# Kernel optimization log

Measured on AMD Instinct MI355X. Metric: run time of the kernel, lower is better.

Reference implementation:

```python
import jax, jax.numpy as jnp
import numpy as np

B, S, HID, H, D = 4, 1024, 2048, 16, 128
ROT = D // 2  # GLM 2D rotary: rotary dim is half the head dim (64)


def _rope_tables(seq_len, dim, base=10000.0):
    # dim = ROT; inv_freq over dim//2 frequencies, emb = cat(freqs, freqs)
    inv_freq = 1.0 / (base ** (jnp.arange(0, dim, 2, dtype=jnp.float32) / dim))
    t = jnp.arange(seq_len, dtype=jnp.float32)
    freqs = jnp.einsum('s,f->sf', t, inv_freq)          # [S, dim//2]
    emb = jnp.concatenate([freqs, freqs], axis=-1)       # [S, dim]
    return jnp.cos(emb), jnp.sin(emb)


def _rotate_half(x):
    x1, x2 = jnp.split(x, 2, axis=-1)
    return jnp.concatenate([-x2, x1], axis=-1)


def _apply_rope(x, cos, sin, pos_id):
    # x: [B,H,S,ROT]; pos_id: [B,S]; tables: [S,ROT]
    c = cos[pos_id][:, None, :, :]  # [B,1,S,ROT]
    s = sin[pos_id][:, None, :, :]
    return x * c + _rotate_half(x) * s


def setup_inputs() -> dict:
    key = jax.random.key(0)
    ks = jax.random.split(key, 12)
    w = 0.02
    inp = {
        'query': jax.random.normal(ks[0], (B, S, HID), jnp.float32),
        'key': jax.random.normal(ks[1], (B, S, HID), jnp.float32),
        'value': jax.random.normal(ks[2], (B, S, HID), jnp.float32),
        'mask': jnp.zeros((B, 1, S, S), jnp.float32),
        'position_bias': jax.random.normal(ks[3], (1, H, S, S), jnp.float32) * 0.1,
        'prev_attn': jax.random.normal(ks[4], (B, H, S, S), jnp.float32) * 0.1,
        'position_ids': jax.random.randint(ks[5], (B, 2, S), 0, S, jnp.int32),
        'Wq': jax.random.normal(ks[6], (HID, HID), jnp.float32) * w,
        'bq': jnp.zeros((HID,), jnp.float32),
        'Wk': jax.random.normal(ks[7], (HID, HID), jnp.float32) * w,
        'bk': jnp.zeros((HID,), jnp.float32),
        'Wv': jax.random.normal(ks[8], (HID, HID), jnp.float32) * w,
        'bv': jnp.zeros((HID,), jnp.float32),
        'Wo': jax.random.normal(ks[9], (HID, HID), jnp.float32) * w,
        'bo': jnp.zeros((HID,), jnp.float32),
    }
    return inp


def reference(query, key, value, mask, position_bias, prev_attn,
              Wq, bq, Wk, bk, Wv, bv, Wo, bo, position_ids):
    # QKV projections -> [B,H,S,D]
    def proj(x, W, b):
        return (x @ W.T + b).reshape(B, S, H, D).transpose(0, 2, 1, 3)
    q = proj(query, Wq, bq)
    k = proj(key, Wk, bk)
    v = proj(value, Wv, bv)

    # GLM 2D rotary: split head dim in halves, rope each with its own ids
    q1, q2 = jnp.split(q, 2, axis=-1)
    k1, k2 = jnp.split(k, 2, axis=-1)
    cos, sin = _rope_tables(S, ROT)
    pid = position_ids[:, 0, :]        # [B,S]
    bid = position_ids[:, 1, :]        # [B,S]
    q1 = _apply_rope(q1, cos, sin, pid)
    k1 = _apply_rope(k1, cos, sin, pid)
    q2 = _apply_rope(q2, cos, sin, bid)
    k2 = _apply_rope(k2, cos, sin, bid)
    q = jnp.concatenate([q1, q2], axis=-1)
    k = jnp.concatenate([k1, k2], axis=-1)

    scores = jnp.einsum('bhsd,bhtd->bhst', q, k)
    scores = scores + position_bias
    scores = scores / jnp.sqrt(jnp.float32(D))
    scores = scores + mask
    scores = scores + prev_attn          # residual attention accumulation
    prev_attn_out = scores
    probs = jax.nn.softmax(scores, axis=-1)
    ctx = jnp.einsum('bhst,bhtd->bhsd', probs, v)
    ctx = ctx.transpose(0, 2, 1, 3).reshape(B, S, HID)
    out = ctx @ Wo.T + bo
    return out, prev_attn_out
```

## Files before the change

kernel.cpp:

```cpp
#include <hip/hip_runtime.h>


#define B_  4
#define S_  1024
#define HID_ 2048
#define H_  16
#define D_  128
#define RSQRT_D 0.08838834764831845f

typedef _Float16 f16x8 __attribute__((ext_vector_type(8)));
typedef _Float16 f16x4 __attribute__((ext_vector_type(4)));
typedef float f32x4 __attribute__((ext_vector_type(4)));
typedef unsigned int u32x2 __attribute__((ext_vector_type(2)));
typedef unsigned int u32x4 __attribute__((ext_vector_type(4)));

#define MFMA16(a, b, c) __builtin_amdgcn_mfma_f32_16x16x32_f16(a, b, c, 0, 0, 0)

__device__ __forceinline__ void gll16(const void* g, void* l) {
  __builtin_amdgcn_global_load_lds(
      (const __attribute__((address_space(1))) void*)g,
      (__attribute__((address_space(3))) void*)l, 16, 0, 0);
}

__global__ __launch_bounds__(256) void cvt_all_kernel(
    const float* __restrict__ w0, const float* __restrict__ w1,
    const float* __restrict__ w2, const float* __restrict__ w3,
    const float* __restrict__ x0, const float* __restrict__ x1,
    const float* __restrict__ x2,
    _Float16* __restrict__ dw0, _Float16* __restrict__ dw1,
    _Float16* __restrict__ dw2, _Float16* __restrict__ dw3,
    _Float16* __restrict__ dx0, _Float16* __restrict__ dx1,
    _Float16* __restrict__ dx2,
    float* __restrict__ tcos, float* __restrict__ tsin) {
  if (blockIdx.x >= 20480) {
    const int i = (blockIdx.x - 20480) * 256 + threadIdx.x;
    const int pos = i >> 5, j = i & 31;
    const float inv = expf(-(float)j * (9.210340371976184f / 32.0f));
    const float ang = (float)pos * inv;
    tcos[i] = cosf(ang);
    tsin[i] = sinf(ang);
    return;
  }
  const int i = blockIdx.x * blockDim.x + threadIdx.x;
  const float* src;
  _Float16* dst;
  int off;
  if (i < 2097152) {
    const int seg = i >> 19;
    off = i & 524287;
    src = (seg == 0) ? w0 : (seg == 1) ? w1 : (seg == 2) ? w2 : w3;
    dst = (seg == 0) ? dw0 : (seg == 1) ? dw1 : (seg == 2) ? dw2 : dw3;
  } else {
    const int j = i - 2097152;
    const int seg = j >> 20;
    off = j & 1048575;
    src = (seg == 0) ? x0 : (seg == 1) ? x1 : x2;
    dst = (seg == 0) ? dx0 : (seg == 1) ? dx1 : dx2;
  }
  const f32x4* in4 = (const f32x4*)src;
  f32x4 a = in4[(size_t)off * 2], b = in4[(size_t)off * 2 + 1];
  f16x8 v;
  v[0] = (_Float16)a[0]; v[1] = (_Float16)a[1]; v[2] = (_Float16)a[2]; v[3] = (_Float16)a[3];
  v[4] = (_Float16)b[0]; v[5] = (_Float16)b[1]; v[6] = (_Float16)b[2]; v[7] = (_Float16)b[3];
  *(f16x8*)(dst + (size_t)off * 8) = v;
}

__global__ __launch_bounds__(256) void proj_qkv_kernel(
    const _Float16* __restrict__ Xq, const _Float16* __restrict__ Xk,
    const _Float16* __restrict__ Xv,
    const _Float16* __restrict__ Wq, const _Float16* __restrict__ Wk,
    const _Float16* __restrict__ Wv,
    const float* __restrict__ bq, const float* __restrict__ bk,
    const float* __restrict__ bv,
    _Float16* __restrict__ oq, _Float16* __restrict__ ok,
    _Float16* __restrict__ ovt,
    const int* __restrict__ pids, const float* __restrict__ tcos,
    const float* __restrict__ tsin) {
  constexpr int N = HID_, K = HID_;
  constexpr int BK = 64;
  __shared__ _Float16 As[128 * BK];
  __shared__ _Float16 Bs[128 * BK];

  const int tid = threadIdx.x;
  const int gbid = (blockIdx.x & 7) * 192 + (blockIdx.x >> 3);
  const int seg = gbid >> 9;
  const int bid = gbid & 511;
  const _Float16* A  = (seg == 0) ? Xq : (seg == 1) ? Xk : Xv;
  const _Float16* Bw = (seg == 0) ? Wq : (seg == 1) ? Wk : Wv;
  const float*  bias = (seg == 0) ? bq : (seg == 1) ? bk : bv;

  const int tm = bid >> 4, tn = bid & 15;
  const int m0 = tm * 128, n0 = tn * 128;
  const int w = tid >> 6, l = tid & 63;
  const int mw = (w >> 1) * 64, nw = (w & 1) * 64;
  const int lr = l & 15, lh = l >> 4;

  f32x4 acc[4][4] = {};

  for (int kt = 0; kt < K / BK; ++kt) {
    const int k0 = kt * BK;
    __syncthreads();
#pragma unroll
    for (int i = 0; i < 4; ++i) {
      const int e = i * 2048 + tid * 8;
      gll16(A + (size_t)(m0 + (e >> 6)) * K + k0 + (e & 63), As + e);
      gll16(Bw + (size_t)(n0 + (e >> 6)) * K + k0 + (e & 63), Bs + e);
    }
    asm volatile("s_waitcnt vmcnt(0)" ::: "memory");
    __syncthreads();
#pragma unroll
    for (int kk = 0; kk < 2; ++kk) {
      f16x8 af[4], bf[4];
#pragma unroll
      for (int mi = 0; mi < 4; ++mi)
        af[mi] = *(const f16x8*)(As + (mw + mi * 16 + lr) * BK + kk * 32 + lh * 8);
#pragma unroll
      for (int ni = 0; ni < 4; ++ni)
        bf[ni] = *(const f16x8*)(Bs + (nw + ni * 16 + lr) * BK + kk * 32 + lh * 8);
#pragma unroll
      for (int mi = 0; mi < 4; ++mi)
#pragma unroll
        for (int ni = 0; ni < 4; ++ni)
          acc[mi][ni] = MFMA16(af[mi], bf[ni], acc[mi][ni]);
    }
  }

  if (seg == 2) {
    _Float16* out = ovt;
#pragma unroll
    for (int mi = 0; mi < 4; ++mi)
#pragma unroll
      for (int ni = 0; ni < 4; ++ni) {
        const int col = n0 + nw + ni * 16 + lr;
        const float bb = bias[col];
        const int h = col >> 7, hd = col & 127;
#pragma unroll
        for (int r = 0; r < 4; ++r) {
          const int row = m0 + mw + mi * 16 + lh * 4 + r;
          const int b = row >> 10, s = row & 1023;
          out[(((size_t)(b * H_ + h)) * D_ + hd) * S_ + s] = (_Float16)(acc[mi][ni][r] + bb);
        }
      }
  } else {
    _Float16* out = (seg == 0) ? oq : ok;
    const int sel = (nw >> 6) & 1;
#pragma unroll
    for (int mi = 0; mi < 4; ++mi) {
#pragma unroll
      for (int r = 0; r < 4; ++r) {
        const int row = m0 + mw + mi * 16 + lh * 4 + r;
        const int b = row >> 10, s = row & 1023;
        const int pos = pids[b * 2 * S_ + sel * S_ + s];
#pragma unroll
        for (int ni = 0; ni < 2; ++ni) {
          const int col = n0 + nw + ni * 16 + lr;
          const int j = ni * 16 + lr;
          const float c = tcos[pos * 32 + j];
          const float sn = tsin[pos * 32 + j];
          const float x1 = acc[mi][ni][r] + bias[col];
          const float x2 = acc[mi][ni + 2][r] + bias[col + 32];
          const int h = col >> 7, hd = col & 127;
          const size_t base = (((size_t)(b * H_ + h)) * S_ + s) * D_;
          out[base + hd] = (_Float16)(x1 * c - x2 * sn);
          out[base + hd + 32] = (_Float16)(x2 * c + x1 * sn);
        }
      }
    }
  }
}

__global__ __launch_bounds__(256) void proj_out_kernel(
    const _Float16* __restrict__ A, const _Float16* __restrict__ Bw,
    const float* __restrict__ bias, float* __restrict__ out) {
  constexpr int N = HID_, K = HID_;
  constexpr int BK = 64;
  __shared__ _Float16 As[128 * BK];
  __shared__ _Float16 Bs[128 * BK];

  const int tid = threadIdx.x;
  const int bid = (blockIdx.x & 7) * 64 + (blockIdx.x >> 3);
  const int tm = bid >> 4, tn = bid & 15;
  const int m0 = tm * 128, n0 = tn * 128;
  const int w = tid >> 6, l = tid & 63;
  const int mw = (w >> 1) * 64, nw = (w & 1) * 64;
  const int lr = l & 15, lh = l >> 4;

  f32x4 acc[4][4] = {};

  for (int kt = 0; kt < K / BK; ++kt) {
    const int k0 = kt * BK;
    __syncthreads();
#pragma unroll
    for (int i = 0; i < 4; ++i) {
      const int e = i * 2048 + tid * 8;
      gll16(A + (size_t)(m0 + (e >> 6)) * K + k0 + (e & 63), As + e);
      gll16(Bw + (size_t)(n0 + (e >> 6)) * K + k0 + (e & 63), Bs + e);
    }
    asm volatile("s_waitcnt vmcnt(0)" ::: "memory");
    __syncthreads();
#pragma unroll
    for (int kk = 0; kk < 2; ++kk) {
      f16x8 af[4], bf[4];
#pragma unroll
      for (int mi = 0; mi < 4; ++mi)
        af[mi] = *(const f16x8*)(As + (mw + mi * 16 + lr) * BK + kk * 32 + lh * 8);
#pragma unroll
      for (int ni = 0; ni < 4; ++ni)
        bf[ni] = *(const f16x8*)(Bs + (nw + ni * 16 + lr) * BK + kk * 32 + lh * 8);
#pragma unroll
      for (int mi = 0; mi < 4; ++mi)
#pragma unroll
        for (int ni = 0; ni < 4; ++ni)
          acc[mi][ni] = MFMA16(af[mi], bf[ni], acc[mi][ni]);
    }
  }

#pragma unroll
  for (int mi = 0; mi < 4; ++mi)
#pragma unroll
    for (int ni = 0; ni < 4; ++ni) {
      const int col = n0 + nw + ni * 16 + lr;
      const float bb = bias[col];
#pragma unroll
      for (int r = 0; r < 4; ++r) {
        const int row = m0 + mw + mi * 16 + lh * 4 + r;
        out[(size_t)row * N + col] = acc[mi][ni][r] + bb;
      }
    }
}

__global__ __launch_bounds__(256) void flash_kernel(
    const _Float16* __restrict__ q, const _Float16* __restrict__ k,
    const _Float16* __restrict__ vt, const float* __restrict__ pbias,
    const float* __restrict__ maskp, const float* __restrict__ prev,
    float* __restrict__ scores, _Float16* __restrict__ ctx) {
  constexpr int BT = 64;
  __shared__ _Float16 Ks[BT * D_];
  __shared__ _Float16 VTs[D_ * BT];

  const int tid = threadIdx.x, w = tid >> 6, l = tid & 63;
  const int lr = l & 15, lh = l >> 4;
  const int sid = (blockIdx.x & 7) * 128 + (blockIdx.x >> 3);
  const int qt = sid & 15, byh = sid >> 4;
  const int b = byh >> 4, h = byh & 15;
  const size_t plane = (size_t)byh;
  const int q0 = qt * 64 + w * 16;
  const int qrow = q0 + lr;
  const int swz = (lr & 7) << 3;

  const int srcA = lr + ((l & 16) << 1);
  const int srcB = srcA + 16;
  const bool selHi = (l & 32) != 0;

  const float* prow  = prev  + (plane * S_ + qrow) * S_;
  const float* pbrow = pbias + ((size_t)h * S_ + qrow) * S_;
  const float* mrow  = maskp + ((size_t)b * S_ + qrow) * S_;
  float*       srow  = scores + (plane * S_ + qrow) * S_;
  const _Float16* kpl = k  + plane * S_ * D_;
  const _Float16* vpl = vt + plane * D_ * S_;

  f16x8 qa[4];
#pragma unroll
  for (int kk = 0; kk < 4; ++kk)
    qa[kk] = *(const f16x8*)(q + (plane * S_ + qrow) * D_ + kk * 32 + lh * 8);

  f32x4 o[8] = {};
  float m_r = -1e30f, l_r = 0.0f;

  for (int tt = 0; tt < S_ / BT; ++tt) {
    const int t0 = tt * BT;

    f32x4 pv4[4], pb4[4], mk4[4];
#pragma unroll
    for (int nt = 0; nt < 4; ++nt) {
      const int toff = t0 + nt * 16 + lh * 4;
      pv4[nt] = *(const f32x4*)(prow + toff);
      pb4[nt] = *(const f32x4*)(pbrow + toff);
      mk4[nt] = *(const f32x4*)(mrow + toff);
    }
#pragma unroll
    for (int i = 0; i < 4; ++i) {
      const int e = i * 2048 + tid * 8;
      const int krow = e >> 7;
      gll16(kpl + (size_t)(t0 + krow) * D_ + ((e & 127) ^ ((krow & 7) << 3)), Ks + e);
      const int vrow = e >> 6;
      gll16(vpl + (size_t)vrow * S_ + t0 + ((e & 63) ^ ((vrow & 7) << 3)), VTs + e);
    }
    __syncthreads();

    f32x4 sa[4] = {};
    __builtin_amdgcn_s_setprio(1);
#pragma unroll
    for (int nt = 0; nt < 4; ++nt)
#pragma unroll
      for (int kk = 0; kk < 4; ++kk) {
        const int row = nt * 16 + lr;
        f16x8 kb = *(const f16x8*)(Ks + row * D_ + ((kk * 32 + lh * 8) ^ swz));
        sa[nt] = MFMA16(kb, qa[kk], sa[nt]);
      }
    __builtin_amdgcn_s_setprio(0);

#pragma unroll
    for (int nt = 0; nt < 4; ++nt) {
      const int toff = t0 + nt * 16 + lh * 4;
      f32x4 sc4 = (sa[nt] + pb4[nt]) * RSQRT_D + mk4[nt] + pv4[nt];
      *(f32x4*)(srow + toff) = sc4;
      sa[nt] = sc4;
    }

    float tmx = -1e30f;
#pragma unroll
    for (int nt = 0; nt < 4; ++nt)
#pragma unroll
      for (int r = 0; r < 4; ++r) tmx = fmaxf(tmx, sa[nt][r]);
    tmx = fmaxf(tmx, __shfl_xor(tmx, 16));
    tmx = fmaxf(tmx, __shfl_xor(tmx, 32));
    if (!__all(tmx <= m_r + 8.0f)) {
      const float newm = fmaxf(m_r, tmx);
      const float al = __expf(m_r - newm);
      m_r = newm;
      l_r *= al;
#pragma unroll
      for (int nd = 0; nd < 8; ++nd) o[nd] *= al;
    }
    float ts = 0.0f;
#pragma unroll
    for (int nt = 0; nt < 4; ++nt)
#pragma unroll
      for (int r = 0; r < 4; ++r) {
        const float pe = __expf(sa[nt][r] - m_r);
        sa[nt][r] = pe;
        ts += pe;
      }
    ts += __shfl_xor(ts, 16);
    ts += __shfl_xor(ts, 32);
    l_r += ts;

    unsigned int u0w0, u0w1, u1w0, u1w1, u2w0, u2w1, u3w0, u3w1;
    {
      f16x4 pk0, pk1, pk2, pk3;
#pragma unroll
      for (int r = 0; r < 4; ++r) {
        pk0[r] = (_Float16)sa[0][r]; pk1[r] = (_Float16)sa[1][r];
        pk2[r] = (_Float16)sa[2][r]; pk3[r] = (_Float16)sa[3][r];
      }
      u32x2 v0 = __builtin_bit_cast(u32x2, pk0); u0w0 = v0[0]; u0w1 = v0[1];
      u32x2 v1 = __builtin_bit_cast(u32x2, pk1); u1w0 = v1[0]; u1w1 = v1[1];
      u32x2 v2 = __builtin_bit_cast(u32x2, pk2); u2w0 = v2[0]; u2w1 = v2[1];
      u32x2 v3 = __builtin_bit_cast(u32x2, pk3); u3w0 = v3[0]; u3w1 = v3[1];
    }
    const unsigned a00 = (unsigned)__shfl((int)u0w0, srcA), a01 = (unsigned)__shfl((int)u0w1, srcA);
    const unsigned a10 = (unsigned)__shfl((int)u1w0, srcA), a11 = (unsigned)__shfl((int)u1w1, srcA);
    const unsigned a20 = (unsigned)__shfl((int)u2w0, srcA), a21 = (unsigned)__shfl((int)u2w1, srcA);
    const unsigned a30 = (unsigned)__shfl((int)u3w0, srcA), a31 = (unsigned)__shfl((int)u3w1, srcA);
    const unsigned b00 = (unsigned)__shfl((int)u0w0, srcB), b01 = (unsigned)__shfl((int)u0w1, srcB);
    const unsigned b10 = (unsigned)__shfl((int)u1w0, srcB), b11 = (unsigned)__shfl((int)u1w1, srcB);
    const unsigned b20 = (unsigned)__shfl((int)u2w0, srcB), b21 = (unsigned)__shfl((int)u2w1, srcB);
    const unsigned b30 = (unsigned)__shfl((int)u3w0, srcB), b31 = (unsigned)__shfl((int)u3w1, srcB);
    u32x4 paw0, paw1;
    paw0[0] = selHi ? a10 : a00; paw0[1] = selHi ? a11 : a01;
    paw0[2] = selHi ? b10 : b00; paw0[3] = selHi ? b11 : b01;
    paw1[0] = selHi ? a30 : a20; paw1[1] = selHi ? a31 : a21;
    paw1[2] = selHi ? b30 : b20; paw1[3] = selHi ? b31 : b21;
    const f16x8 pa0 = __builtin_bit_cast(f16x8, paw0);
    const f16x8 pa1 = __builtin_bit_cast(f16x8, paw1);

    __builtin_amdgcn_s_setprio(1);
#pragma unroll
    for (int nd = 0; nd < 8; ++nd) {
      const int vr = nd * 16 + lr;
      const f16x8 vb0 = *(const f16x8*)(VTs + vr * BT + ((lh * 8) ^ swz));
      o[nd] = MFMA16(vb0, pa0, o[nd]);
    }
#pragma unroll
    for (int nd = 0; nd < 8; ++nd) {
      const int vr = nd * 16 + lr;
      const f16x8 vb1 = *(const f16x8*)(VTs + vr * BT + ((32 + lh * 8) ^ swz));
      o[nd] = MFMA16(vb1, pa1, o[nd]);
    }
    __builtin_amdgcn_s_setprio(0);

    __builtin_amdgcn_s_barrier();
  }

  const float inv_l = 1.0f / l_r;
  _Float16* crow = ctx + ((size_t)(b * S_) + qrow) * HID_ + h * D_;
#pragma unroll
  for (int nd = 0; nd < 8; ++nd) {
    f16x4 cv;
#pragma unroll
    for (int r = 0; r < 4; ++r) cv[r] = (_Float16)(o[nd][r] * inv_l);
    *(f16x4*)(crow + nd * 16 + lh * 4) = cv;
  }
}

extern "C" void kernel_launch(void* const* d_in, const int* in_sizes, int n_in,
                              void* d_out, int out_size, void* d_ws, size_t ws_size,
                              hipStream_t stream) {
  const float* query = (const float*)d_in[0];
  const float* key_i = (const float*)d_in[1];
  const float* value = (const float*)d_in[2];
  const float* maskp = (const float*)d_in[3];
  const float* pbias = (const float*)d_in[4];
  const float* prev  = (const float*)d_in[5];
  const int*   pids  = (const int*)d_in[6];
  const float* Wq = (const float*)d_in[7];
  const float* bq = (const float*)d_in[8];
  const float* Wk = (const float*)d_in[9];
  const float* bk = (const float*)d_in[10];
  const float* Wv = (const float*)d_in[11];
  const float* bv = (const float*)d_in[12];
  const float* Wo = (const float*)d_in[13];
  const float* bo = (const float*)d_in[14];

  char* ws = (char*)d_ws;
  const size_t OFF_TCOS = 0;
  const size_t OFF_TSIN = 131072;
  const size_t OFF_W    = 262144;
  const size_t OFF_X    = OFF_W + 4ull * 8388608;
  const size_t OFF_Q    = OFF_X + 3ull * 16777216;
  const size_t OFF_K    = OFF_Q + 16777216;
  const size_t OFF_VT   = OFF_K + 16777216;
  const size_t OFF_CTX  = OFF_X + 16777216;

  float* tcos = (float*)(ws + OFF_TCOS);
  float* tsin = (float*)(ws + OFF_TSIN);
  _Float16* Wq16 = (_Float16*)(ws + OFF_W);
  _Float16* Wk16 = (_Float16*)(ws + OFF_W + 8388608);
  _Float16* Wv16 = (_Float16*)(ws + OFF_W + 2ull * 8388608);
  _Float16* Wo16 = (_Float16*)(ws + OFF_W + 3ull * 8388608);
  _Float16* Xq16 = (_Float16*)(ws + OFF_X);
  _Float16* Xk16 = (_Float16*)(ws + OFF_X + 16777216);
  _Float16* Xv16 = (_Float16*)(ws + OFF_X + 2ull * 16777216);
  _Float16* q16  = (_Float16*)(ws + OFF_Q);
  _Float16* k16  = (_Float16*)(ws + OFF_K);
  _Float16* vt16 = (_Float16*)(ws + OFF_VT);
  _Float16* ctx16 = (_Float16*)(ws + OFF_CTX);

  float* out_f32 = (float*)d_out;
  float* scores  = (float*)d_out + 8388608;

  cvt_all_kernel<<<20608, 256, 0, stream>>>(Wq, Wk, Wv, Wo, query, key_i, value,
                                            Wq16, Wk16, Wv16, Wo16,
                                            Xq16, Xk16, Xv16, tcos, tsin);

  proj_qkv_kernel<<<1536, 256, 0, stream>>>(Xq16, Xk16, Xv16,
                                            Wq16, Wk16, Wv16,
                                            bq, bk, bv,
                                            q16, k16, vt16,
                                            pids, tcos, tsin);

  flash_kernel<<<1024, 256, 0, stream>>>(q16, k16, vt16, pbias, maskp, prev,
                                         scores, ctx16);

  proj_out_kernel<<<512, 256, 0, stream>>>(ctx16, Wo16, bo, out_f32);
}
```

Before: 474.1 us.

## Double-buffer per-wave K/V tiles in flash kernel and drop block barriers

The flash attention loop now gives each wave its own private, double-buffered LDS copy of the K and V^T tiles, with the key tile width halved from 64 to 32. The next tile's K/V and its bias, mask and prev_attn rows are prefetched while the current tile is computed, using an explicit vmcnt wait in place of __syncthreads and the trailing barrier. The goal is to remove block-wide synchronisation and hide global load latency. In exchange, each wave loads the full tiles redundantly (four times the LDS fill traffic), LDS use grows to about 128 KB per block, and occupancy drops.

```diff
diff --git a/kernel.cpp b/kernel.cpp
--- a/kernel.cpp
+++ b/kernel.cpp
@@ -234,9 +234,9 @@
     const _Float16* __restrict__ vt, const float* __restrict__ pbias,
     const float* __restrict__ maskp, const float* __restrict__ prev,
     float* __restrict__ scores, _Float16* __restrict__ ctx) {
-  constexpr int BT = 64;
-  __shared__ _Float16 Ks[BT * D_];
-  __shared__ _Float16 VTs[D_ * BT];
+  constexpr int BT = 32;
+  __shared__ _Float16 KsAll[4][2][BT * D_];
+  __shared__ _Float16 VTsAll[4][2][D_ * BT];
 
   const int tid = threadIdx.x, w = tid >> 6, l = tid & 63;
   const int lr = l & 15, lh = l >> 4;
@@ -267,52 +267,75 @@
   f32x4 o[8] = {};
   float m_r = -1e30f, l_r = 0.0f;
 
+  _Float16* kA = &KsAll[w][0][0];
+  _Float16* kB = &KsAll[w][1][0];
+  _Float16* vA = &VTsAll[w][0][0];
+  _Float16* vB = &VTsAll[w][1][0];
+
+  f32x4 pvA[2], pbA[2], mkA[2];
+#pragma unroll
+  for (int nt = 0; nt < 2; ++nt) {
+    const int toff = nt * 16 + lh * 4;
+    pvA[nt] = *(const f32x4*)(prow + toff);
+    pbA[nt] = *(const f32x4*)(pbrow + toff);
+    mkA[nt] = *(const f32x4*)(mrow + toff);
+  }
+#pragma unroll
+  for (int i = 0; i < 8; ++i) {
+    const int e = i * 512 + l * 8;
+    const int krow = e >> 7;
+    gll16(kpl + (size_t)krow * D_ + ((e & 127) ^ ((krow & 7) << 3)), kA + e);
+    const int vrow = e >> 5;
+    gll16(vpl + (size_t)vrow * S_ + ((e & 31) ^ (((vrow >> 1) & 3) << 3)), vA + e);
+  }
+  asm volatile("s_waitcnt vmcnt(0)" ::: "memory");
+  __builtin_amdgcn_sched_barrier(0);
+
   for (int tt = 0; tt < S_ / BT; ++tt) {
     const int t0 = tt * BT;
-
-    f32x4 pv4[4], pb4[4], mk4[4];
-#pragma unroll
-    for (int nt = 0; nt < 4; ++nt) {
-      const int toff = t0 + nt * 16 + lh * 4;
-      pv4[nt] = *(const f32x4*)(prow + toff);
-      pb4[nt] = *(const f32x4*)(pbrow + toff);
-      mk4[nt] = *(const f32x4*)(mrow + toff);
-    }
-#pragma unroll
-    for (int i = 0; i < 4; ++i) {
-      const int e = i * 2048 + tid * 8;
+    const int t1 = (tt < S_ / BT - 1) ? t0 + BT : 0;
+
+    f32x4 pvB[2], pbB[2], mkB[2];
+#pragma unroll
+    for (int nt = 0; nt < 2; ++nt) {
+      const int toff = t1 + nt * 16 + lh * 4;
+      pvB[nt] = *(const f32x4*)(prow + toff);
+      pbB[nt] = *(const f32x4*)(pbrow + toff);
+      mkB[nt] = *(const f32x4*)(mrow + toff);
+    }
+#pragma unroll
+    for (int i = 0; i < 8; ++i) {
+      const int e = i * 512 + l * 8;
       const int krow = e >> 7;
-      gll16(kpl + (size_t)(t0 + krow) * D_ + ((e & 127) ^ ((krow & 7) << 3)), Ks + e);
-      const int vrow = e >> 6;
-      gll16(vpl + (size_t)vrow * S_ + t0 + ((e & 63) ^ ((vrow & 7) << 3)), VTs + e);
-    }
-    __syncthreads();
-
-    f32x4 sa[4] = {};
+      gll16(kpl + (size_t)(t1 + krow) * D_ + ((e & 127) ^ ((krow & 7) << 3)), kB + e);
+      const int vrow = e >> 5;
+      gll16(vpl + (size_t)vrow * S_ + t1 + ((e & 31) ^ (((vrow >> 1) & 3) << 3)), vB + e);
+    }
+    asm volatile("s_waitcnt vmcnt(24)" ::: "memory");
+    __builtin_amdgcn_sched_barrier(0);
+
+    f32x4 sa[2] = {};
     __builtin_amdgcn_s_setprio(1);
 #pragma unroll
-    for (int nt = 0; nt < 4; ++nt)
+    for (int nt = 0; nt < 2; ++nt)
 #pragma unroll
       for (int kk = 0; kk < 4; ++kk) {
         const int row = nt * 16 + lr;
-        f16x8 kb = *(const f16x8*)(Ks + row * D_ + ((kk * 32 + lh * 8) ^ swz));
+        f16x8 kb = *(const f16x8*)(kA + row * D_ + ((kk * 32 + lh * 8) ^ swz));
         sa[nt] = MFMA16(kb, qa[kk], sa[nt]);
       }
     __builtin_amdgcn_s_setprio(0);
 
 #pragma unroll
-    for (int nt = 0; nt < 4; ++nt) {
+    for (int nt = 0; nt < 2; ++nt) {
       const int toff = t0 + nt * 16 + lh * 4;
-      f32x4 sc4 = (sa[nt] + pb4[nt]) * RSQRT_D + mk4[nt] + pv4[nt];
+      f32x4 sc4 = (sa[nt] + pbA[nt]) * RSQRT_D + mkA[nt] + pvA[nt];
       *(f32x4*)(srow + toff) = sc4;
       sa[nt] = sc4;
     }
 
-    float tmx = -1e30f;
-#pragma unroll
-    for (int nt = 0; nt < 4; ++nt)
-#pragma unroll
-      for (int r = 0; r < 4; ++r) tmx = fmaxf(tmx, sa[nt][r]);
+    float tmx = fmaxf(fmaxf(fmaxf(sa[0][0], sa[0][1]), fmaxf(sa[0][2], sa[0][3])),
+                      fmaxf(fmaxf(sa[1][0], sa[1][1]), fmaxf(sa[1][2], sa[1][3])));
     tmx = fmaxf(tmx, __shfl_xor(tmx, 16));
     tmx = fmaxf(tmx, __shfl_xor(tmx, 32));
     if (!__all(tmx <= m_r + 8.0f)) {
@@ -325,7 +348,7 @@
     }
     float ts = 0.0f;
 #pragma unroll
-    for (int nt = 0; nt < 4; ++nt)
+    for (int nt = 0; nt < 2; ++nt)
 #pragma unroll
       for (int r = 0; r < 4; ++r) {
         const float pe = __expf(sa[nt][r] - m_r);
@@ -336,51 +359,39 @@
     ts += __shfl_xor(ts, 32);
     l_r += ts;
 
-    unsigned int u0w0, u0w1, u1w0, u1w1, u2w0, u2w1, u3w0, u3w1;
+    unsigned int u0w0, u0w1, u1w0, u1w1;
     {
-      f16x4 pk0, pk1, pk2, pk3;
-#pragma unroll
-      for (int r = 0; r < 4; ++r) {
-        pk0[r] = (_Float16)sa[0][r]; pk1[r] = (_Float16)sa[1][r];
-        pk2[r] = (_Float16)sa[2][r]; pk3[r] = (_Float16)sa[3][r];
-      }
+      f16x4 pk0, pk1;
+#pragma unroll
+      for (int r = 0; r < 4; ++r) { pk0[r] = (_Float16)sa[0][r]; pk1[r] = (_Float16)sa[1][r]; }
       u32x2 v0 = __builtin_bit_cast(u32x2, pk0); u0w0 = v0[0]; u0w1 = v0[1];
       u32x2 v1 = __builtin_bit_cast(u32x2, pk1); u1w0 = v1[0]; u1w1 = v1[1];
-      u32x2 v2 = __builtin_bit_cast(u32x2, pk2); u2w0 = v2[0]; u2w1 = v2[1];
-      u32x2 v3 = __builtin_bit_cast(u32x2, pk3); u3w0 = v3[0]; u3w1 = v3[1];
     }
     const unsigned a00 = (unsigned)__shfl((int)u0w0, srcA), a01 = (unsigned)__shfl((int)u0w1, srcA);
     const unsigned a10 = (unsigned)__shfl((int)u1w0, srcA), a11 = (unsigned)__shfl((int)u1w1, srcA);
-    const unsigned a20 = (unsigned)__shfl((int)u2w0, srcA), a21 = (unsigned)__shfl((int)u2w1, srcA);
-    const unsigned a30 = (unsigned)__shfl((int)u3w0, srcA), a31 = (unsigned)__shfl((int)u3w1, srcA);
     const unsigned b00 = (unsigned)__shfl((int)u0w0, srcB), b01 = (unsigned)__shfl((int)u0w1, srcB);
     const unsigned b10 = (unsigned)__shfl((int)u1w0, srcB), b11 = (unsigned)__shfl((int)u1w1, srcB);
-    const unsigned b20 = (unsigned)__shfl((int)u2w0, srcB), b21 = (unsigned)__shfl((int)u2w1, srcB);
-    const unsigned b30 = (unsigned)__shfl((int)u3w0, srcB), b31 = (unsigned)__shfl((int)u3w1, srcB);
-    u32x4 paw0, paw1;
-    paw0[0] = selHi ? a10 : a00; paw0[1] = selHi ? a11 : a01;
-    paw0[2] = selHi ? b10 : b00; paw0[3] = selHi ? b11 : b01;
-    paw1[0] = selHi ? a30 : a20; paw1[1] = selHi ? a31 : a21;
-    paw1[2] = selHi ? b30 : b20; paw1[3] = selHi ? b31 : b21;
-    const f16x8 pa0 = __builtin_bit_cast(f16x8, paw0);
-    const f16x8 pa1 = __builtin_bit_cast(f16x8, paw1);
+    u32x4 paw;
+    paw[0] = selHi ? a10 : a00; paw[1] = selHi ? a11 : a01;
+    paw[2] = selHi ? b10 : b00; paw[3] = selHi ? b11 : b01;
+    const f16x8 pa = __builtin_bit_cast(f16x8, paw);
 
     __builtin_amdgcn_s_setprio(1);
 #pragma unroll
     for (int nd = 0; nd < 8; ++nd) {
       const int vr = nd * 16 + lr;
-      const f16x8 vb0 = *(const f16x8*)(VTs + vr * BT + ((lh * 8) ^ swz));
-      o[nd] = MFMA16(vb0, pa0, o[nd]);
-    }
-#pragma unroll
-    for (int nd = 0; nd < 8; ++nd) {
-      const int vr = nd * 16 + lr;
-      const f16x8 vb1 = *(const f16x8*)(VTs + vr * BT + ((32 + lh * 8) ^ swz));
-      o[nd] = MFMA16(vb1, pa1, o[nd]);
+      const f16x8 vb = *(const f16x8*)(vA + vr * BT + ((lh * 8) ^ (((vr >> 1) & 3) << 3)));
+      o[nd] = MFMA16(vb, pa, o[nd]);
     }
     __builtin_amdgcn_s_setprio(0);
 
-    __builtin_amdgcn_s_barrier();
+    _Float16* tp;
+    tp = kA; kA = kB; kB = tp;
+    tp = vA; vA = vB; vB = tp;
+#pragma unroll
+    for (int nt = 0; nt < 2; ++nt) {
+      pvA[nt] = pvB[nt]; pbA[nt] = pbB[nt]; mkA[nt] = mkB[nt];
+    }
   }
 
   const float inv_l = 1.0f / l_r;
```

Result: slower. 569.2 us (+20.1%).
